# Performance work log

Measured on AMD Instinct MI355X. Metric: run time of the kernel, lower is better.

Reference implementation:

```python
import jax, jax.numpy as jnp
import numpy as np

BETA = 1.0  # init_kwargs beta

B, D, N = 8, 3, 4096
LATENT = 256

def setup_inputs() -> dict:
    key = jax.random.key(0)
    k1, k2, k3, k4 = jax.random.split(key, 4)
    return {
        "recon_x": jax.random.normal(k1, (B, D, N), dtype=jnp.float32),
        "x": jax.random.normal(k2, (B, D, N), dtype=jnp.float32),
        "mu": jax.random.normal(k3, (B, LATENT), dtype=jnp.float32),
        "logvar": jax.random.normal(k4, (B, LATENT), dtype=jnp.float32),
    }

def _chamfer(xc, yc):
    # xc, yc: [B, D, N] channels-first point clouds -> [B, N, D]
    xp = jnp.swapaxes(xc, 2, 1)  # [B, N, D]
    yp = jnp.swapaxes(yc, 2, 1)  # [B, M, D]
    # squared L2 pairwise distances via gram expansion (avoids [B,N,M,D] intermediate)
    x2 = jnp.sum(xp * xp, axis=-1)               # [B, N]
    y2 = jnp.sum(yp * yp, axis=-1)               # [B, M]
    xy = jnp.einsum("bnd,bmd->bnm", xp, yp)      # [B, N, M]
    dist = x2[:, :, None] + y2[:, None, :] - 2.0 * xy  # [B, N, M]
    min_x = jnp.min(dist, axis=2)  # [B, N] nearest y for each x
    min_y = jnp.min(dist, axis=1)  # [B, M] nearest x for each y
    return jnp.mean(min_x) + jnp.mean(min_y)

def _kl(mu, logvar):
    kld = -0.5 * jnp.sum(1.0 + logvar - mu * mu - jnp.exp(logvar))
    return kld / mu.shape[0]

def reference(recon_x, x, mu, logvar):
    recon_loss = _chamfer(recon_x, x)
    kld_loss = _kl(mu, logvar)
    total_loss = recon_loss + BETA * kld_loss
    return (total_loss, recon_loss, kld_loss)
```

## Files before the change

### kernel.cpp

```cpp
#include <hip/hip_runtime.h>
#include <math.h>

#define BB 8
#define NN 4096
#define LATENT 256

#define THREADS 256
#define P 8
#define CSPLIT 64
#define TT (NN / CSPLIT)
#define NSLOTS (2 * BB * NN)
#define BLOCKS_X (2 * BB)

__device__ __forceinline__ unsigned enc(float f) {
    unsigned b = __float_as_uint(f);
    return (b & 0x80000000u) ? ~b : (b | 0x80000000u);
}
__device__ __forceinline__ float dec(unsigned k) {
    unsigned b = (k & 0x80000000u) ? (k ^ 0x80000000u) : ~k;
    return __uint_as_float(b);
}

__device__ __forceinline__ float min3f(float a, float b, float c) {
    float d;
    asm("v_min3_f32 %0, %1, %2, %3" : "=v"(d) : "v"(a), "v"(b), "v"(c));
    return d;
}

__device__ __forceinline__ float2 dist_pk(float2 cxy, float2 czw,
                                          float2 qx, float2 qy, float2 qz) {
    float2 t;
    asm("v_pk_fma_f32 %0, %1, %2, %1 op_sel:[0,0,1] op_sel_hi:[0,1,1]"
        : "=v"(t) : "v"(czw), "v"(qz));
    asm("v_pk_fma_f32 %0, %1, %2, %0 op_sel:[1,0,0] op_sel_hi:[1,1,1]"
        : "+v"(t) : "v"(cxy), "v"(qy));
    asm("v_pk_fma_f32 %0, %1, %2, %0 op_sel:[0,0,0] op_sel_hi:[0,1,1]"
        : "+v"(t) : "v"(cxy), "v"(qx));
    return t;
}

__global__ __launch_bounds__(THREADS)
void init_kernel(unsigned* __restrict__ minkeys, unsigned* __restrict__ counter)
{
    int i = blockIdx.x * THREADS + threadIdx.x;
    minkeys[i] = 0xFFFFFFFFu;
    if (i == 0) *counter = 0u;
}

__global__ __launch_bounds__(THREADS, 4)
void chamfer_stage1(const float* __restrict__ recon,
                    const float* __restrict__ x,
                    unsigned* __restrict__ minkeys)
{
    __shared__ float4 ly[TT];

    const int bx  = blockIdx.x;
    const int c   = blockIdx.y;
    const int dir = bx >> 3;
    const int b   = bx & 7;
    const int tid = threadIdx.x;

    const float* cloud = (dir ? recon : x) + (size_t)b * 3 * NN;
    const float* query = (dir ? x : recon) + (size_t)b * 3 * NN;

    if (tid < TT) {
        int m = c * TT + tid;
        float y0 = cloud[m];
        float y1 = cloud[NN + m];
        float y2 = cloud[2 * NN + m];
        ly[tid] = make_float4(-2.0f * y0, -2.0f * y1, -2.0f * y2,
                              y0 * y0 + y1 * y1 + y2 * y2);
    }
    __syncthreads();

    float2 qx[P], qy[P], qz[P];
    float mn0[P], mn1[P];
#pragma unroll
    for (int p = 0; p < P; ++p) {
        int ql = p * THREADS + tid;
        int qh = ql + 2048;
        qx[p] = make_float2(query[ql],          query[qh]);
        qy[p] = make_float2(query[NN + ql],     query[NN + qh]);
        qz[p] = make_float2(query[2 * NN + ql], query[2 * NN + qh]);
        mn0[p] = 3.4e38f;
        mn1[p] = 3.4e38f;
    }

#pragma unroll 4
    for (int j = 0; j < TT; j += 2) {
        float4 A = ly[j];
        float4 B = ly[j + 1];
        float2 Axy = make_float2(A.x, A.y), Azw = make_float2(A.z, A.w);
        float2 Bxy = make_float2(B.x, B.y), Bzw = make_float2(B.z, B.w);
#pragma unroll
        for (int p = 0; p < P; ++p) {
            float2 ta = dist_pk(Axy, Azw, qx[p], qy[p], qz[p]);
            float2 tb = dist_pk(Bxy, Bzw, qx[p], qy[p], qz[p]);
            mn0[p] = min3f(mn0[p], ta.x, tb.x);
            mn1[p] = min3f(mn1[p], ta.y, tb.y);
        }
    }

    const int base = dir * (BB * NN) + b * NN;
#pragma unroll
    for (int p = 0; p < P; ++p) {
        int ql = p * THREADS + tid;
        int qh = ql + 2048;
        float sx0 = fmaf(qx[p].x, qx[p].x, fmaf(qy[p].x, qy[p].x, qz[p].x * qz[p].x));
        float sx1 = fmaf(qx[p].y, qx[p].y, fmaf(qy[p].y, qy[p].y, qz[p].y * qz[p].y));
        atomicMin(&minkeys[base + ql], enc(sx0 + mn0[p]));
        atomicMin(&minkeys[base + qh], enc(sx1 + mn1[p]));
    }
}

__global__ __launch_bounds__(THREADS)
void chamfer_stage2(const unsigned* __restrict__ minkeys,
                    const float* __restrict__ mu,
                    const float* __restrict__ logvar,
                    float* __restrict__ sums,
                    unsigned* __restrict__ counter,
                    float* __restrict__ out)
{
    __shared__ float red[4];
    __shared__ float redA[4];
    __shared__ float redB[4];
    __shared__ int amLast;

    const int tid = threadIdx.x;
    const int bid = blockIdx.x;

    float v = dec(minkeys[bid * THREADS + tid]);
    for (int off = 32; off > 0; off >>= 1)
        v += __shfl_down(v, off);
    if ((tid & 63) == 0) red[tid >> 6] = v;
    __syncthreads();

    if (tid == 0) {
        float tot = red[0] + red[1] + red[2] + red[3];
        __hip_atomic_store(&sums[bid], tot, __ATOMIC_RELEASE, __HIP_MEMORY_SCOPE_AGENT);
        unsigned old = __hip_atomic_fetch_add(counter, 1u, __ATOMIC_ACQ_REL, __HIP_MEMORY_SCOPE_AGENT);
        amLast = (old == 255u);
    }
    __syncthreads();
    if (!amLast) return;

    float s = __hip_atomic_load(&sums[tid], __ATOMIC_ACQUIRE, __HIP_MEMORY_SCOPE_AGENT);

    float kl = 0.0f;
    for (int i = tid; i < BB * LATENT; i += THREADS) {
        float m  = mu[i];
        float lv = logvar[i];
        kl += 1.0f + lv - m * m - expf(lv);
    }

    for (int off = 32; off > 0; off >>= 1) {
        s  += __shfl_down(s, off);
        kl += __shfl_down(kl, off);
    }
    if ((tid & 63) == 0) { redA[tid >> 6] = s; redB[tid >> 6] = kl; }
    __syncthreads();
    if (tid == 0) {
        float recon = (redA[0] + redA[1] + redA[2] + redA[3]) / (float)(BB * NN);
        float kld   = -0.5f * (redB[0] + redB[1] + redB[2] + redB[3]) / (float)BB;
        out[0] = recon + kld;
        out[1] = recon;
        out[2] = kld;
    }
}

extern "C" void kernel_launch(void* const* d_in, const int* in_sizes, int n_in,
                              void* d_out, int out_size, void* d_ws, size_t ws_size,
                              hipStream_t stream)
{
    const float* recon  = (const float*)d_in[0];
    const float* x      = (const float*)d_in[1];
    const float* mu     = (const float*)d_in[2];
    const float* logvar = (const float*)d_in[3];
    float* out = (float*)d_out;

    unsigned* minkeys = (unsigned*)d_ws;
    float*    sums    = (float*)(minkeys + NSLOTS);
    unsigned* counter = (unsigned*)(sums + 256);

    init_kernel<<<NSLOTS / THREADS, THREADS, 0, stream>>>(minkeys, counter);

    dim3 g1(BLOCKS_X, CSPLIT);
    chamfer_stage1<<<g1, THREADS, 0, stream>>>(recon, x, minkeys);

    chamfer_stage2<<<NSLOTS / THREADS, THREADS, 0, stream>>>(minkeys, mu, logvar,
                                                             sums, counter, out);
}
```

Baseline: 43.77 us.

## Replace atomicMin reduction with per-chunk partial minima and drop init kernel

Stage 1 now writes each block's per-query minimum to a dedicated slice of a partial buffer instead of doing encoded atomicMin, so the init kernel disappears and the counter is reset inside stage 1. The grid is also re-split: queries are tiled into two halves per batch and cloud chunks are halved (CSPLIT 32), giving 32x32 blocks with fewer registers per thread. Stage 2 reduces across the 32 partial slices before the sum. This removes one launch and the atomic traffic, at the cost of a 4 MB partial write and read.

```diff
diff --git a/kernel.cpp b/kernel.cpp
--- a/kernel.cpp
+++ b/kernel.cpp
@@ -6,20 +6,13 @@
 #define LATENT 256
 
 #define THREADS 256
-#define P 8
-#define CSPLIT 64
+#define QP 4
+#define QBLK (THREADS * QP * 2)
+#define QTILES (NN / QBLK)
+#define CSPLIT 32
 #define TT (NN / CSPLIT)
 #define NSLOTS (2 * BB * NN)
-#define BLOCKS_X (2 * BB)
-
-__device__ __forceinline__ unsigned enc(float f) {
-    unsigned b = __float_as_uint(f);
-    return (b & 0x80000000u) ? ~b : (b | 0x80000000u);
-}
-__device__ __forceinline__ float dec(unsigned k) {
-    unsigned b = (k & 0x80000000u) ? (k ^ 0x80000000u) : ~k;
-    return __uint_as_float(b);
-}
+#define BLOCKS_X (2 * BB * QTILES)
 
 __device__ __forceinline__ float min3f(float a, float b, float c) {
     float d;
@@ -39,46 +32,44 @@
     return t;
 }
 
-__global__ __launch_bounds__(THREADS)
-void init_kernel(unsigned* __restrict__ minkeys, unsigned* __restrict__ counter)
-{
-    int i = blockIdx.x * THREADS + threadIdx.x;
-    minkeys[i] = 0xFFFFFFFFu;
-    if (i == 0) *counter = 0u;
-}
-
 __global__ __launch_bounds__(THREADS, 4)
 void chamfer_stage1(const float* __restrict__ recon,
                     const float* __restrict__ x,
-                    unsigned* __restrict__ minkeys)
+                    float* __restrict__ partial,
+                    unsigned* __restrict__ counter)
 {
     __shared__ float4 ly[TT];
 
     const int bx  = blockIdx.x;
     const int c   = blockIdx.y;
-    const int dir = bx >> 3;
-    const int b   = bx & 7;
+    const int dir = bx >> 4;
+    const int rem = bx & 15;
+    const int b   = rem >> 1;
+    const int qt  = rem & 1;
     const int tid = threadIdx.x;
+
+    if (bx == 0 && c == 0 && tid == 0) *counter = 0u;
 
     const float* cloud = (dir ? recon : x) + (size_t)b * 3 * NN;
     const float* query = (dir ? x : recon) + (size_t)b * 3 * NN;
 
-    if (tid < TT) {
-        int m = c * TT + tid;
+    for (int i = tid; i < TT; i += THREADS) {
+        int m = c * TT + i;
         float y0 = cloud[m];
         float y1 = cloud[NN + m];
         float y2 = cloud[2 * NN + m];
-        ly[tid] = make_float4(-2.0f * y0, -2.0f * y1, -2.0f * y2,
-                              y0 * y0 + y1 * y1 + y2 * y2);
+        ly[i] = make_float4(-2.0f * y0, -2.0f * y1, -2.0f * y2,
+                            y0 * y0 + y1 * y1 + y2 * y2);
     }
     __syncthreads();
 
-    float2 qx[P], qy[P], qz[P];
-    float mn0[P], mn1[P];
+    const int q0 = qt * QBLK + tid;
+    float2 qx[QP], qy[QP], qz[QP];
+    float mn0[QP], mn1[QP];
 #pragma unroll
-    for (int p = 0; p < P; ++p) {
-        int ql = p * THREADS + tid;
-        int qh = ql + 2048;
+    for (int p = 0; p < QP; ++p) {
+        int ql = q0 + p * THREADS;
+        int qh = ql + (QBLK / 2);
         qx[p] = make_float2(query[ql],          query[qh]);
         qy[p] = make_float2(query[NN + ql],     query[NN + qh]);
         qz[p] = make_float2(query[2 * NN + ql], query[2 * NN + qh]);
@@ -86,14 +77,14 @@
         mn1[p] = 3.4e38f;
     }
 
-#pragma unroll 4
+#pragma unroll 2
     for (int j = 0; j < TT; j += 2) {
         float4 A = ly[j];
         float4 B = ly[j + 1];
         float2 Axy = make_float2(A.x, A.y), Azw = make_float2(A.z, A.w);
         float2 Bxy = make_float2(B.x, B.y), Bzw = make_float2(B.z, B.w);
 #pragma unroll
-        for (int p = 0; p < P; ++p) {
+        for (int p = 0; p < QP; ++p) {
             float2 ta = dist_pk(Axy, Azw, qx[p], qy[p], qz[p]);
             float2 tb = dist_pk(Bxy, Bzw, qx[p], qy[p], qz[p]);
             mn0[p] = min3f(mn0[p], ta.x, tb.x);
@@ -101,20 +92,20 @@
         }
     }
 
-    const int base = dir * (BB * NN) + b * NN;
+    float* dst = partial + (size_t)c * NSLOTS + dir * (BB * NN) + b * NN;
 #pragma unroll
-    for (int p = 0; p < P; ++p) {
-        int ql = p * THREADS + tid;
-        int qh = ql + 2048;
+    for (int p = 0; p < QP; ++p) {
+        int ql = q0 + p * THREADS;
+        int qh = ql + (QBLK / 2);
         float sx0 = fmaf(qx[p].x, qx[p].x, fmaf(qy[p].x, qy[p].x, qz[p].x * qz[p].x));
         float sx1 = fmaf(qx[p].y, qx[p].y, fmaf(qy[p].y, qy[p].y, qz[p].y * qz[p].y));
-        atomicMin(&minkeys[base + ql], enc(sx0 + mn0[p]));
-        atomicMin(&minkeys[base + qh], enc(sx1 + mn1[p]));
+        dst[ql] = sx0 + mn0[p];
+        dst[qh] = sx1 + mn1[p];
     }
 }
 
 __global__ __launch_bounds__(THREADS)
-void chamfer_stage2(const unsigned* __restrict__ minkeys,
+void chamfer_stage2(const float* __restrict__ partial,
                     const float* __restrict__ mu,
                     const float* __restrict__ logvar,
                     float* __restrict__ sums,
@@ -128,8 +119,18 @@
 
     const int tid = threadIdx.x;
     const int bid = blockIdx.x;
+    const int gq  = bid * THREADS + tid;
 
-    float v = dec(minkeys[bid * THREADS + tid]);
+    float m0 = partial[gq];
+    float m1 = partial[(size_t)1 * NSLOTS + gq];
+    for (int cc = 2; cc < CSPLIT; cc += 2) {
+        float a = partial[(size_t)cc * NSLOTS + gq];
+        float b = partial[(size_t)(cc + 1) * NSLOTS + gq];
+        m0 = fminf(m0, a);
+        m1 = fminf(m1, b);
+    }
+    float v = fminf(m0, m1);
+
     for (int off = 32; off > 0; off >>= 1)
         v += __shfl_down(v, off);
     if ((tid & 63) == 0) red[tid >> 6] = v;
@@ -178,15 +179,12 @@
     const float* logvar = (const float*)d_in[3];
     float* out = (float*)d_out;
 
-    unsigned* minkeys = (unsigned*)d_ws;
-    float*    sums    = (float*)(minkeys + NSLOTS);
+    float*    partial = (float*)d_ws;
+    float*    sums    = partial + (size_t)CSPLIT * NSLOTS;
     unsigned* counter = (unsigned*)(sums + 256);
 
-    init_kernel<<<NSLOTS / THREADS, THREADS, 0, stream>>>(minkeys, counter);
-
     dim3 g1(BLOCKS_X, CSPLIT);
-    chamfer_stage1<<<g1, THREADS, 0, stream>>>(recon, x, minkeys);
-
-    chamfer_stage2<<<NSLOTS / THREADS, THREADS, 0, stream>>>(minkeys, mu, logvar,
+    chamfer_stage1<<<g1, THREADS, 0, stream>>>(recon, x, partial, counter);
+    chamfer_stage2<<<NSLOTS / THREADS, THREADS, 0, stream>>>(partial, mu, logvar,
                                                              sums, counter, out);
 }
```

Result: faster. 39.50 us (-9.8%).
